# Optimization experiments

Measured on AMD Instinct MI355X. Metric: run time of the kernel, lower is better.

## Reference

```python
import jax, jax.numpy as jnp
import numpy as np

C, H, W = 128, 128, 128
N_LINES = 8192
N_POINTS = 32
POOL = 4
DIM_FC = 1024


def setup_inputs() -> dict:
    key = jax.random.key(0)
    ks = jax.random.split(key, 8)
    feats = jax.random.normal(ks[0], (C, H, W), dtype=jnp.float32)
    # line endpoints (x1,y1,x2,y2) in feature-map pixel coords
    lines = jax.random.uniform(ks[1], (N_LINES, 4), dtype=jnp.float32) * (H - 1)
    d_in = C * (N_POINTS // POOL)  # 1024
    W1 = jax.random.normal(ks[2], (DIM_FC, d_in), dtype=jnp.float32) * 0.02
    b1 = jax.random.normal(ks[3], (DIM_FC,), dtype=jnp.float32) * 0.02
    W2 = jax.random.normal(ks[4], (DIM_FC, DIM_FC), dtype=jnp.float32) * 0.02
    b2 = jax.random.normal(ks[5], (DIM_FC,), dtype=jnp.float32) * 0.02
    W3 = jax.random.normal(ks[6], (4, DIM_FC), dtype=jnp.float32) * 0.02
    b3 = jax.random.normal(ks[7], (4,), dtype=jnp.float32) * 0.02
    return {
        "features_per_image": feats,
        "lines_per_im": lines,
        "W1": W1, "b1": b1, "W2": W2, "b2": b2, "W3": W3, "b3": b3,
        "n_points": N_POINTS,
        "pool_stride": POOL,
    }


def _extract_pt_feats(features, lines, n_points):
    # features: [C, H, W]; lines: [N, 4]
    c, h, w = features.shape
    tspan = jnp.linspace(0.0, 1.0, n_points).astype(features.dtype)  # [P]
    U, V = lines[:, :2], lines[:, 2:]
    # [N, 2, P] -> interpolate endpoints, shift by 0.5 (torch pixel-center convention)
    pts = U[:, :, None] * tspan + V[:, :, None] * (1.0 - tspan) - 0.5
    pts = pts.transpose(0, 2, 1).reshape(-1, 2)  # [N*P, 2]
    px, py = pts[:, 0], pts[:, 1]
    # NOTE: faithful to torch source: px indexes the h-axis but is clamped with w-1,
    # py indexes the w-axis but is clamped with h-1 (harmless here since H == W).
    px0 = jnp.clip(jnp.floor(px), 0.0, w - 1)
    py0 = jnp.clip(jnp.floor(py), 0.0, h - 1)
    px1 = jnp.clip(px0 + 1.0, 0.0, w - 1)
    py1 = jnp.clip(py0 + 1.0, 0.0, h - 1)
    px0i, py0i = px0.astype(jnp.int32), py0.astype(jnp.int32)
    px1i, py1i = px1.astype(jnp.int32), py1.astype(jnp.int32)
    # four irregular gathers + bilinear weights, fused expression. each term: [C, N*P]
    xp = (features[:, px0i, py0i] * ((py1 - py) * (px1 - px))
          + features[:, px0i, py1i] * ((py - py0) * (px1 - px))
          + features[:, px1i, py0i] * ((py1 - py) * (px - px0))
          + features[:, px1i, py1i] * ((py - py0) * (px - px0)))
    return xp.reshape(c, -1, n_points).transpose(1, 0, 2)  # [N, C, P]


def reference(features_per_image, lines_per_im, W1, b1, W2, b2, W3, b3,
              n_points, pool_stride):
    xp = _extract_pt_feats(features_per_image, lines_per_im, n_points)  # [N, C, P]
    n, c, p = xp.shape
    # MaxPool1d(kernel=stride=pool_stride)
    pooled = xp.reshape(n, c, p // pool_stride, pool_stride).max(axis=-1)
    flat = pooled.reshape(n, -1)  # [N, C*(P//s)]
    h1 = jax.nn.relu(flat @ W1.T + b1)
    h2 = jax.nn.relu(h1 @ W2.T + b2)
    return h2 @ W3.T + b3  # [N, 4]
```

## Files before the change

kernel.cpp:

```cpp
#include <hip/hip_runtime.h>
#include <hip/hip_bf16.h>
#include <cstdint>

typedef __attribute__((ext_vector_type(4))) float f32x4;
typedef __attribute__((ext_vector_type(8))) short short8;

#define DEVI __device__ __forceinline__

DEVI uint16_t f2bf(float v) {
    union { float f; uint32_t u; } c; c.f = v;
    uint32_t u = c.u + 0x7FFFu + ((c.u >> 16) & 1u);
    return (uint16_t)(u >> 16);
}
DEVI float bflo(uint32_t u) { union { uint32_t u; float f; } c; c.u = u << 16; return c.f; }
DEVI float bfhi(uint32_t u) { union { uint32_t u; float f; } c; c.u = u & 0xFFFF0000u; return c.f; }

DEVI void async16(const uint16_t* g, uint16_t* l) {
    __builtin_amdgcn_global_load_lds((const __attribute__((address_space(1))) void*)g,
                                     (__attribute__((address_space(3))) void*)l, 16, 0, 0);
}

__global__ __launch_bounds__(256) void init_out(float* __restrict__ out, const float* __restrict__ b3) {
    const int i = blockIdx.x * 256 + threadIdx.x;
    float4 b = { b3[0], b3[1], b3[2], b3[3] };
    ((float4*)out)[i] = b;
}

__global__ __launch_bounds__(256) void prep_all(const float* __restrict__ f, uint16_t* __restrict__ featT,
                                                const float* __restrict__ W1, uint16_t* __restrict__ W1b,
                                                const float* __restrict__ W2, uint16_t* __restrict__ W2b) {
    if (blockIdx.x < 128) {
        __shared__ uint16_t s[128 * 130];
        const int x = blockIdx.x;
        const float* fx = f + x * 128;
        for (int i = threadIdx.x; i < 16384; i += 256) {
            int c = i >> 7, y = i & 127;
            s[y * 130 + c] = f2bf(fx[c * 16384 + y]);
        }
        __syncthreads();
        uint16_t* o = featT + x * 16384;
        for (int i = threadIdx.x; i < 16384; i += 256) {
            int y = i >> 7, c = i & 127;
            o[i] = s[y * 130 + c];
        }
    } else {
        const int i = (blockIdx.x - 128) * 256 + threadIdx.x;
        float4 a = ((const float4*)W1)[i];
        float4 b = ((const float4*)W2)[i];
        ushort4 pa = { f2bf(a.x), f2bf(a.y), f2bf(a.z), f2bf(a.w) };
        ushort4 pb = { f2bf(b.x), f2bf(b.y), f2bf(b.z), f2bf(b.w) };
        ((ushort4*)W1b)[i] = pa;
        ((ushort4*)W2b)[i] = pb;
    }
}

__global__ __launch_bounds__(256) void extract_k(const float4* __restrict__ lines,
                                                 const uint16_t* __restrict__ featT,
                                                 uint16_t* __restrict__ flat) {
    const int n = blockIdx.x;
    const int tid = threadIdx.x;
    const int lane = tid & 63, wave = tid >> 6;
    const float4 ln = lines[n];
    __shared__ uint16_t ps[1024];
    const uint16_t* fb = featT + lane * 2;

    for (int g2 = 0; g2 < 2; ++g2) {
        const int g = wave * 2 + g2;
        float m0 = -1e30f, m1 = -1e30f;
#pragma unroll
        for (int pp = 0; pp < 4; ++pp) {
            const float t = (float)(g * 4 + pp) * (1.0f / 31.0f);
            const float x = ln.x * t + ln.z * (1.0f - t) - 0.5f;
            const float y = ln.y * t + ln.w * (1.0f - t) - 0.5f;
            const float x0f = fminf(fmaxf(floorf(x), 0.0f), 127.0f);
            const float y0f = fminf(fmaxf(floorf(y), 0.0f), 127.0f);
            const float x1f = fminf(x0f + 1.0f, 127.0f);
            const float y1f = fminf(y0f + 1.0f, 127.0f);
            const int x0 = (int)x0f, x1 = (int)x1f, y0 = (int)y0f, y1 = (int)y1f;
            const float wx1 = x - x0f, wx0 = x1f - x;
            const float wy1 = y - y0f, wy0 = y1f - y;
            const uint32_t u00 = *(const uint32_t*)(fb + ((x0 * 128 + y0) << 7));
            const uint32_t u01 = *(const uint32_t*)(fb + ((x0 * 128 + y1) << 7));
            const uint32_t u10 = *(const uint32_t*)(fb + ((x1 * 128 + y0) << 7));
            const uint32_t u11 = *(const uint32_t*)(fb + ((x1 * 128 + y1) << 7));
            const float w00 = wy0 * wx0, w01 = wy1 * wx0, w10 = wy0 * wx1, w11 = wy1 * wx1;
            const float a = bflo(u00) * w00 + bflo(u01) * w01 + bflo(u10) * w10 + bflo(u11) * w11;
            const float b = bfhi(u00) * w00 + bfhi(u01) * w01 + bfhi(u10) * w10 + bfhi(u11) * w11;
            m0 = fmaxf(m0, a);
            m1 = fmaxf(m1, b);
        }
        ps[lane * 16 + g]     = f2bf(m0);
        ps[lane * 16 + 8 + g] = f2bf(m1);
    }
    __syncthreads();
    *(uint2*)(flat + (size_t)n * 1024 + tid * 4) = ((const uint2*)ps)[tid];
}

template <int FUSE3>
__global__ __launch_bounds__(256) void gemm_bt(const uint16_t* __restrict__ A,
                                               const uint16_t* __restrict__ B,
                                               const float* __restrict__ bias,
                                               uint16_t* __restrict__ Co,
                                               const float* __restrict__ W3,
                                               float* __restrict__ out3,
                                               int M, int N, int K) {
    __shared__ uint16_t As[128 * 32];
    __shared__ uint16_t Bs[128 * 32];
    const int tid = threadIdx.x;
    const int lane = tid & 63, wave = tid >> 6;
    const int nbm = M >> 7;
    const int bm = blockIdx.x % nbm;
    const int bn = blockIdx.x / nbm;
    const int wr = wave >> 1, wc = wave & 1;
    const int l15 = lane & 15, l16 = lane >> 4;

    f32x4 acc[4][4] = {};

    const uint16_t* Ag = A + (size_t)(bm * 128) * K;
    const uint16_t* Bg = B + (size_t)(bn * 128) * K;

    for (int kt = 0; kt < K; kt += 32) {
        if (kt) __syncthreads();
#pragma unroll
        for (int i = 0; i < 2; ++i) {
            const int c = i * 256 + tid;
            const int row = c >> 2, slot = c & 3;
            const int src = slot ^ ((row >> 1) & 3);
            async16(Ag + (size_t)row * K + kt + src * 8, &As[c * 8]);
            async16(Bg + (size_t)row * K + kt + src * 8, &Bs[c * 8]);
        }
        __syncthreads();
        short8 a[4], b[4];
#pragma unroll
        for (int fm = 0; fm < 4; ++fm) {
            const int r = wr * 64 + fm * 16 + l15;
            a[fm] = *(const short8*)&As[r * 32 + (l16 ^ ((r >> 1) & 3)) * 8];
        }
#pragma unroll
        for (int fn = 0; fn < 4; ++fn) {
            const int r = wc * 64 + fn * 16 + l15;
            b[fn] = *(const short8*)&Bs[r * 32 + (l16 ^ ((r >> 1) & 3)) * 8];
        }
#pragma unroll
        for (int fm = 0; fm < 4; ++fm)
#pragma unroll
            for (int fn = 0; fn < 4; ++fn)
                acc[fm][fn] = __builtin_amdgcn_mfma_f32_16x16x32_bf16(a[fm], b[fn], acc[fm][fn], 0, 0, 0);
    }

    if (!FUSE3) {
#pragma unroll
        for (int fm = 0; fm < 4; ++fm) {
            const int row = bm * 128 + wr * 64 + fm * 16 + l16 * 4;
#pragma unroll
            for (int fn = 0; fn < 4; ++fn) {
                const int col = bn * 128 + wc * 64 + fn * 16 + l15;
                const float bv = bias[col];
#pragma unroll
                for (int r = 0; r < 4; ++r) {
                    float v = fmaxf(acc[fm][fn][r] + bv, 0.0f);
                    Co[(size_t)(row + r) * N + col] = f2bf(v);
                }
            }
        }
    } else {
        float bv[4], w3v[4][4];
#pragma unroll
        for (int fn = 0; fn < 4; ++fn) {
            const int col = bn * 128 + wc * 64 + fn * 16 + l15;
            bv[fn] = bias[col];
#pragma unroll
            for (int j = 0; j < 4; ++j) w3v[j][fn] = W3[j * N + col];
        }
#pragma unroll
        for (int fm = 0; fm < 4; ++fm) {
            const int row = bm * 128 + wr * 64 + fm * 16 + l16 * 4;
#pragma unroll
            for (int r = 0; r < 4; ++r) {
                float p[4] = { 0.0f, 0.0f, 0.0f, 0.0f };
#pragma unroll
                for (int fn = 0; fn < 4; ++fn) {
                    const float hv = fmaxf(acc[fm][fn][r] + bv[fn], 0.0f);
#pragma unroll
                    for (int j = 0; j < 4; ++j) p[j] += hv * w3v[j][fn];
                }
#pragma unroll
                for (int off = 1; off <= 8; off <<= 1)
#pragma unroll
                    for (int j = 0; j < 4; ++j) p[j] += __shfl_xor(p[j], off);
                if (l15 == 0) {
                    float* o = out3 + (size_t)(row + r) * 4;
#pragma unroll
                    for (int j = 0; j < 4; ++j) atomicAdd(o + j, p[j]);
                }
            }
        }
    }
}

extern "C" void kernel_launch(void* const* d_in, const int* in_sizes, int n_in,
                              void* d_out, int out_size, void* d_ws, size_t ws_size,
                              hipStream_t stream) {
    const float* feats = (const float*)d_in[0];
    const float* lines = (const float*)d_in[1];
    const float* W1 = (const float*)d_in[2];
    const float* b1 = (const float*)d_in[3];
    const float* W2 = (const float*)d_in[4];
    const float* b2 = (const float*)d_in[5];
    const float* W3 = (const float*)d_in[6];
    const float* b3 = (const float*)d_in[7];
    float* out = (float*)d_out;

    char* ws = (char*)d_ws;
    uint16_t* featT = (uint16_t*)(ws);
    uint16_t* W1b   = (uint16_t*)(ws + (4u << 20));
    uint16_t* W2b   = (uint16_t*)(ws + (6u << 20));
    uint16_t* flat  = (uint16_t*)(ws + (8u << 20));
    uint16_t* h1    = (uint16_t*)(ws + (24u << 20));

    init_out<<<32, 256, 0, stream>>>(out, b3);
    prep_all<<<1152, 256, 0, stream>>>(feats, featT, W1, W1b, W2, W2b);
    extract_k<<<8192, 256, 0, stream>>>((const float4*)lines, featT, flat);
    gemm_bt<0><<<512, 256, 0, stream>>>(flat, W1b, b1, h1, nullptr, nullptr, 8192, 1024, 1024);
    gemm_bt<1><<<512, 256, 0, stream>>>(h1, W2b, b2, nullptr, W3, out, 8192, 1024, 1024);
}
```

Before: 118.0 us.

## Split GEMM K dimension across two wave groups with LDS reduction

Each GEMM block now runs 512 threads as two 256-thread groups, each covering half of K with its own LDS tile buffers, and the partial accumulators are then summed through shared memory before the epilogue. The goal is more waves per block to hide load latency, since the grid of 512 blocks only lightly fills the GPU. The cost is twice the LDS per block, extra barriers in the reduction loop, and an idle half-block during the epilogue.

```diff
diff --git a/kernel.cpp b/kernel.cpp
--- a/kernel.cpp
+++ b/kernel.cpp
@@ -96,50 +96,60 @@
     *(uint2*)(flat + (size_t)n * 1024 + tid * 4) = ((const uint2*)ps)[tid];
 }
 
+
+DEVI void stage_swz(const uint16_t* Ag, const uint16_t* Bg, int K, int ktAbs,
+                    uint16_t* as, uint16_t* bs, int t256) {
+#pragma unroll
+    for (int i = 0; i < 2; ++i) {
+        const int c = i * 256 + t256;
+        const int row = c >> 2, slot = c & 3;
+        const int src = slot ^ ((row >> 1) & 3);
+        async16(Ag + (size_t)row * K + ktAbs + src * 8, as + c * 8);
+        async16(Bg + (size_t)row * K + ktAbs + src * 8, bs + c * 8);
+    }
+}
+
 template <int FUSE3>
-__global__ __launch_bounds__(256) void gemm_bt(const uint16_t* __restrict__ A,
-                                               const uint16_t* __restrict__ B,
-                                               const float* __restrict__ bias,
-                                               uint16_t* __restrict__ Co,
-                                               const float* __restrict__ W3,
-                                               float* __restrict__ out3,
-                                               int M, int N, int K) {
-    __shared__ uint16_t As[128 * 32];
-    __shared__ uint16_t Bs[128 * 32];
+__global__ __launch_bounds__(512, 4) void gemm_bt(const uint16_t* __restrict__ A,
+                                                  const uint16_t* __restrict__ B,
+                                                  const float* __restrict__ bias,
+                                                  uint16_t* __restrict__ Co,
+                                                  const float* __restrict__ W3,
+                                                  float* __restrict__ out3,
+                                                  int M, int N, int K) {
+    __shared__ uint16_t As[2][128 * 32];
+    __shared__ uint16_t Bs[2][128 * 32];
     const int tid = threadIdx.x;
-    const int lane = tid & 63, wave = tid >> 6;
+    const int t256 = tid & 255;
+    const int ks = tid >> 8;
+    const int lane = tid & 63;
+    const int w2 = (tid >> 6) & 3;
+    const int wr = w2 >> 1, wc = w2 & 1;
+    const int l15 = lane & 15, l16 = lane >> 4;
     const int nbm = M >> 7;
     const int bm = blockIdx.x % nbm;
     const int bn = blockIdx.x / nbm;
-    const int wr = wave >> 1, wc = wave & 1;
-    const int l15 = lane & 15, l16 = lane >> 4;
 
     f32x4 acc[4][4] = {};
 
     const uint16_t* Ag = A + (size_t)(bm * 128) * K;
     const uint16_t* Bg = B + (size_t)(bn * 128) * K;
-
-    for (int kt = 0; kt < K; kt += 32) {
+    const int kbase = ks * (K >> 1);
+
+    for (int kt = 0; kt < (K >> 1); kt += 32) {
         if (kt) __syncthreads();
-#pragma unroll
-        for (int i = 0; i < 2; ++i) {
-            const int c = i * 256 + tid;
-            const int row = c >> 2, slot = c & 3;
-            const int src = slot ^ ((row >> 1) & 3);
-            async16(Ag + (size_t)row * K + kt + src * 8, &As[c * 8]);
-            async16(Bg + (size_t)row * K + kt + src * 8, &Bs[c * 8]);
-        }
+        stage_swz(Ag, Bg, K, kbase + kt, As[ks], Bs[ks], t256);
         __syncthreads();
         short8 a[4], b[4];
 #pragma unroll
         for (int fm = 0; fm < 4; ++fm) {
             const int r = wr * 64 + fm * 16 + l15;
-            a[fm] = *(const short8*)&As[r * 32 + (l16 ^ ((r >> 1) & 3)) * 8];
+            a[fm] = *(const short8*)&As[ks][r * 32 + (l16 ^ ((r >> 1) & 3)) * 8];
         }
 #pragma unroll
         for (int fn = 0; fn < 4; ++fn) {
             const int r = wc * 64 + fn * 16 + l15;
-            b[fn] = *(const short8*)&Bs[r * 32 + (l16 ^ ((r >> 1) & 3)) * 8];
+            b[fn] = *(const short8*)&Bs[ks][r * 32 + (l16 ^ ((r >> 1) & 3)) * 8];
         }
 #pragma unroll
         for (int fm = 0; fm < 4; ++fm)
@@ -147,6 +157,28 @@
             for (int fn = 0; fn < 4; ++fn)
                 acc[fm][fn] = __builtin_amdgcn_mfma_f32_16x16x32_bf16(a[fm], b[fn], acc[fm][fn], 0, 0, 0);
     }
+
+    float* smemF = (float*)As;
+#pragma unroll
+    for (int fm = 0; fm < 4; ++fm) {
+        __syncthreads();
+        if (ks == 1) {
+#pragma unroll
+            for (int fn = 0; fn < 4; ++fn)
+#pragma unroll
+                for (int r = 0; r < 4; ++r)
+                    smemF[(wr * 16 + l16 * 4 + r) * 128 + wc * 64 + fn * 16 + l15] = acc[fm][fn][r];
+        }
+        __syncthreads();
+        if (ks == 0) {
+#pragma unroll
+            for (int fn = 0; fn < 4; ++fn)
+#pragma unroll
+                for (int r = 0; r < 4; ++r)
+                    acc[fm][fn][r] += smemF[(wr * 16 + l16 * 4 + r) * 128 + wc * 64 + fn * 16 + l15];
+        }
+    }
+    if (ks != 0) return;
 
     if (!FUSE3) {
 #pragma unroll
@@ -221,6 +253,6 @@
     init_out<<<32, 256, 0, stream>>>(out, b3);
     prep_all<<<1152, 256, 0, stream>>>(feats, featT, W1, W1b, W2, W2b);
     extract_k<<<8192, 256, 0, stream>>>((const float4*)lines, featT, flat);
-    gemm_bt<0><<<512, 256, 0, stream>>>(flat, W1b, b1, h1, nullptr, nullptr, 8192, 1024, 1024);
-    gemm_bt<1><<<512, 256, 0, stream>>>(h1, W2b, b2, nullptr, W3, out, 8192, 1024, 1024);
-}
+    gemm_bt<0><<<512, 512, 0, stream>>>(flat, W1b, b1, h1, nullptr, nullptr, 8192, 1024, 1024);
+    gemm_bt<1><<<512, 512, 0, stream>>>(h1, W2b, b2, nullptr, W3, out, 8192, 1024, 1024);
+}
```

Result: faster. 115.3 us (-2.3%).

## Rewrite GEMMs with triple-buffered async LDS pipeline and 256x128 tiles

Applied to the files above, without the earlier changes.

Replaces the single-buffered 128x128 GEMM, which synchronizes on every K=32 step, with a 512-thread 256x128-tile kernel. It uses K=64 slabs held in a three-slot LDS ring, prefetches two slabs ahead, and interleaves global-to-LDS loads with MFMA phases under explicit waitcnt, barriers and setprio. The aim is to hide global load latency behind MFMA work and cut barrier stalls. The cost is 144KB of LDS per block, which limits occupancy. Only 256 blocks are launched per GEMM, which may underfill the device.

```diff
diff --git a/kernel.cpp b/kernel.cpp
--- a/kernel.cpp
+++ b/kernel.cpp
@@ -96,69 +96,129 @@
     *(uint2*)(flat + (size_t)n * 1024 + tid * 4) = ((const uint2*)ps)[tid];
 }
 
+
+DEVI void stage_slab(const uint16_t* Ag, const uint16_t* Bg, int K, int kt,
+                     int s, uint16_t* buf, int tid) {
+    const int c = s * 512 + tid;
+    uint16_t* dst = buf + c * 8;
+    if (s < 4) {
+        const int row = c >> 3, sl = c & 7;
+        async16(Ag + (size_t)row * K + kt + ((sl ^ (row & 7)) << 3), dst);
+    } else {
+        const int c2 = c - 2048;
+        const int row = c2 >> 3, sl = c2 & 7;
+        async16(Bg + (size_t)row * K + kt + ((sl ^ (row & 7)) << 3), dst);
+    }
+}
+
+DEVI void ds_read_phase(const uint16_t* buf, int wr, int wc, int kk,
+                        int l15, int l16, short8* a, short8* b) {
+#pragma unroll
+    for (int rf = 0; rf < 4; ++rf) {
+        const int row = wr * 64 + rf * 16 + l15;
+        a[rf] = *(const short8*)(buf + row * 64 + (((kk * 4 + l16) ^ (row & 7)) << 3));
+    }
+#pragma unroll
+    for (int cf = 0; cf < 4; ++cf) {
+        const int row = wc * 64 + cf * 16 + l15;
+        b[cf] = *(const short8*)(buf + 16384 + row * 64 + (((kk * 4 + l16) ^ (row & 7)) << 3));
+    }
+}
+
 template <int FUSE3>
-__global__ __launch_bounds__(256) void gemm_bt(const uint16_t* __restrict__ A,
-                                               const uint16_t* __restrict__ B,
-                                               const float* __restrict__ bias,
-                                               uint16_t* __restrict__ Co,
-                                               const float* __restrict__ W3,
-                                               float* __restrict__ out3,
-                                               int M, int N, int K) {
-    __shared__ uint16_t As[128 * 32];
-    __shared__ uint16_t Bs[128 * 32];
+__global__ __launch_bounds__(512, 2) void gemm_8ph(const uint16_t* __restrict__ A,
+                                                   const uint16_t* __restrict__ B,
+                                                   const float* __restrict__ bias,
+                                                   uint16_t* __restrict__ Co,
+                                                   const float* __restrict__ W3,
+                                                   float* __restrict__ out3,
+                                                   int M, int N, int K) {
+    __shared__ uint16_t lds3[3][24576];
     const int tid = threadIdx.x;
     const int lane = tid & 63, wave = tid >> 6;
-    const int nbm = M >> 7;
+    const int wr = wave >> 1, wc = wave & 1;
+    const int l15 = lane & 15, l16 = lane >> 4;
+    const int nbm = M >> 8;
     const int bm = blockIdx.x % nbm;
     const int bn = blockIdx.x / nbm;
-    const int wr = wave >> 1, wc = wave & 1;
-    const int l15 = lane & 15, l16 = lane >> 4;
 
     f32x4 acc[4][4] = {};
-
-    const uint16_t* Ag = A + (size_t)(bm * 128) * K;
+    const uint16_t* Ag = A + (size_t)(bm * 256) * K;
     const uint16_t* Bg = B + (size_t)(bn * 128) * K;
-
-    for (int kt = 0; kt < K; kt += 32) {
-        if (kt) __syncthreads();
-#pragma unroll
-        for (int i = 0; i < 2; ++i) {
-            const int c = i * 256 + tid;
-            const int row = c >> 2, slot = c & 3;
-            const int src = slot ^ ((row >> 1) & 3);
-            async16(Ag + (size_t)row * K + kt + src * 8, &As[c * 8]);
-            async16(Bg + (size_t)row * K + kt + src * 8, &Bs[c * 8]);
-        }
-        __syncthreads();
-        short8 a[4], b[4];
-#pragma unroll
-        for (int fm = 0; fm < 4; ++fm) {
-            const int r = wr * 64 + fm * 16 + l15;
-            a[fm] = *(const short8*)&As[r * 32 + (l16 ^ ((r >> 1) & 3)) * 8];
-        }
-#pragma unroll
-        for (int fn = 0; fn < 4; ++fn) {
-            const int r = wc * 64 + fn * 16 + l15;
-            b[fn] = *(const short8*)&Bs[r * 32 + (l16 ^ ((r >> 1) & 3)) * 8];
-        }
-#pragma unroll
-        for (int fm = 0; fm < 4; ++fm)
-#pragma unroll
-            for (int fn = 0; fn < 4; ++fn)
-                acc[fm][fn] = __builtin_amdgcn_mfma_f32_16x16x32_bf16(a[fm], b[fn], acc[fm][fn], 0, 0, 0);
-    }
+    const int NT = K >> 6;
+
+#pragma unroll
+    for (int s = 0; s < 6; ++s) stage_slab(Ag, Bg, K, 0, s, lds3[0], tid);
+#pragma unroll
+    for (int s = 0; s < 6; ++s) stage_slab(Ag, Bg, K, 64, s, lds3[1], tid);
+    asm volatile("s_waitcnt vmcnt(6)" ::: "memory");
+    __builtin_amdgcn_s_barrier();
+
+#define MFMA16(a, b)                                                                  \
+    _Pragma("unroll")                                                                 \
+    for (int rf = 0; rf < 4; ++rf)                                                    \
+        _Pragma("unroll")                                                             \
+        for (int cf = 0; cf < 4; ++cf)                                                \
+            acc[rf][cf] = __builtin_amdgcn_mfma_f32_16x16x32_bf16(a[rf], b[cf], acc[rf][cf], 0, 0, 0);
+
+    int bufi = 0;
+    for (int t = 0; t < NT; ++t) {
+        const uint16_t* buf = lds3[bufi];
+        int wi = bufi + 2; if (wi >= 3) wi -= 3;
+        uint16_t* bufw = lds3[wi];
+        const bool st = (t + 2) < NT;
+        const int ktn = (t + 2) << 6;
+
+        {
+            short8 a[4], b[4];
+            ds_read_phase(buf, wr, wc, 0, l15, l16, a, b);
+            if (st) {
+                stage_slab(Ag, Bg, K, ktn, 0, bufw, tid);
+                stage_slab(Ag, Bg, K, ktn, 1, bufw, tid);
+                stage_slab(Ag, Bg, K, ktn, 2, bufw, tid);
+            }
+            __builtin_amdgcn_s_barrier();
+            asm volatile("s_waitcnt lgkmcnt(0)" ::: "memory");
+            __builtin_amdgcn_sched_barrier(0);
+            __builtin_amdgcn_s_setprio(1);
+            MFMA16(a, b);
+            __builtin_amdgcn_s_setprio(0);
+            __builtin_amdgcn_s_barrier();
+        }
+        {
+            short8 a[4], b[4];
+            ds_read_phase(buf, wr, wc, 1, l15, l16, a, b);
+            if (st) {
+                stage_slab(Ag, Bg, K, ktn, 3, bufw, tid);
+                stage_slab(Ag, Bg, K, ktn, 4, bufw, tid);
+                stage_slab(Ag, Bg, K, ktn, 5, bufw, tid);
+                asm volatile("s_waitcnt vmcnt(6)" ::: "memory");
+            } else {
+                asm volatile("s_waitcnt vmcnt(0)" ::: "memory");
+            }
+            __builtin_amdgcn_s_barrier();
+            asm volatile("s_waitcnt lgkmcnt(0)" ::: "memory");
+            __builtin_amdgcn_sched_barrier(0);
+            __builtin_amdgcn_s_setprio(1);
+            MFMA16(a, b);
+            __builtin_amdgcn_s_setprio(0);
+            __builtin_amdgcn_s_barrier();
+        }
+        bufi = bufi + 1; if (bufi == 3) bufi = 0;
+    }
+#undef MFMA16
 
     if (!FUSE3) {
 #pragma unroll
-        for (int fm = 0; fm < 4; ++fm) {
-            const int row = bm * 128 + wr * 64 + fm * 16 + l16 * 4;
-#pragma unroll
-            for (int fn = 0; fn < 4; ++fn) {
-                const int col = bn * 128 + wc * 64 + fn * 16 + l15;
+        for (int rf = 0; rf < 4; ++rf) {
+            const int row = bm * 256 + wr * 64 + rf * 16 + l16 * 4;
+#pragma unroll
+            for (int cf = 0; cf < 4; ++cf) {
+                const int col = bn * 128 + wc * 64 + cf * 16 + l15;
                 const float bv = bias[col];
 #pragma unroll
                 for (int r = 0; r < 4; ++r) {
-                    float v = fmaxf(acc[fm][fn][r] + bv, 0.0f);
+                    float v = fmaxf(acc[rf][cf][r] + bv, 0.0f);
                     Co[(size_t)(row + r) * N + col] = f2bf(v);
                 }
             }
@@ -166,23 +226,23 @@
     } else {
         float bv[4], w3v[4][4];
 #pragma unroll
-        for (int fn = 0; fn < 4; ++fn) {
-            const int col = bn * 128 + wc * 64 + fn * 16 + l15;
-            bv[fn] = bias[col];
-#pragma unroll
-            for (int j = 0; j < 4; ++j) w3v[j][fn] = W3[j * N + col];
-        }
-#pragma unroll
-        for (int fm = 0; fm < 4; ++fm) {
-            const int row = bm * 128 + wr * 64 + fm * 16 + l16 * 4;
+        for (int cf = 0; cf < 4; ++cf) {
+            const int col = bn * 128 + wc * 64 + cf * 16 + l15;
+            bv[cf] = bias[col];
+#pragma unroll
+            for (int j = 0; j < 4; ++j) w3v[j][cf] = W3[j * N + col];
+        }
+#pragma unroll
+        for (int rf = 0; rf < 4; ++rf) {
+            const int row = bm * 256 + wr * 64 + rf * 16 + l16 * 4;
 #pragma unroll
             for (int r = 0; r < 4; ++r) {
                 float p[4] = { 0.0f, 0.0f, 0.0f, 0.0f };
 #pragma unroll
-                for (int fn = 0; fn < 4; ++fn) {
-                    const float hv = fmaxf(acc[fm][fn][r] + bv[fn], 0.0f);
-#pragma unroll
-                    for (int j = 0; j < 4; ++j) p[j] += hv * w3v[j][fn];
+                for (int cf = 0; cf < 4; ++cf) {
+                    const float hv = fmaxf(acc[rf][cf][r] + bv[cf], 0.0f);
+#pragma unroll
+                    for (int j = 0; j < 4; ++j) p[j] += hv * w3v[j][cf];
                 }
 #pragma unroll
                 for (int off = 1; off <= 8; off <<= 1)
@@ -221,6 +281,6 @@
     init_out<<<32, 256, 0, stream>>>(out, b3);
     prep_all<<<1152, 256, 0, stream>>>(feats, featT, W1, W1b, W2, W2b);
     extract_k<<<8192, 256, 0, stream>>>((const float4*)lines, featT, flat);
-    gemm_bt<0><<<512, 256, 0, stream>>>(flat, W1b, b1, h1, nullptr, nullptr, 8192, 1024, 1024);
-    gemm_bt<1><<<512, 256, 0, stream>>>(h1, W2b, b2, nullptr, W3, out, 8192, 1024, 1024);
-}
+    gemm_8ph<0><<<256, 512, 0, stream>>>(flat, W1b, b1, h1, nullptr, nullptr, 8192, 1024, 1024);
+    gemm_8ph<1><<<256, 512, 0, stream>>>(h1, W2b, b2, nullptr, W3, out, 8192, 1024, 1024);
+}
```

Measured after the change: 131.1 us. +11.1%, slower.
